# Kernel tuning notes

Hardware: AMD Instinct MI355X
Metric: run time of the kernel (lower is better)

Reference implementation:

```python
import jax, jax.numpy as jnp
import numpy as np


def setup_inputs() -> dict:
    key = jax.random.key(0)
    ks = jax.random.split(key, 6)
    B, HW, CIN, COUT, K = 256, 64, 3, 128, 32
    inputs = jax.random.normal(ks[0], (B, HW, HW, CIN), jnp.float32)
    conv_w = jax.random.normal(ks[1], (3, 3, CIN, COUT), jnp.float32) * 0.1
    conv_b = jnp.zeros((COUT,), jnp.float32)
    match_w = jax.random.normal(ks[2], (COUT,), jnp.float32) * 0.1
    match_b = jnp.zeros((1,), jnp.float32)
    pat_w = jax.random.normal(ks[3], (32 * 32 * K, 1), jnp.float32) * 0.01
    pat_b = jnp.zeros((1,), jnp.float32)
    base_w = jax.random.normal(ks[4], (32 * 32 * COUT, 3), jnp.float32) * 0.01
    base_b = jnp.zeros((3,), jnp.float32)
    pattern_set_index = jax.random.randint(ks[5], (K,), 0, COUT, jnp.int32)
    return {
        "inputs": inputs, "conv_w": conv_w, "conv_b": conv_b,
        "match_w": match_w, "match_b": match_b,
        "pat_w": pat_w, "pat_b": pat_b,
        "base_w": base_w, "base_b": base_b,
        "pattern_set_index": pattern_set_index,
    }


def reference(inputs, conv_w, conv_b, match_w, match_b,
              pat_w, pat_b, base_w, base_b, pattern_set_index):
    B = inputs.shape[0]
    # feat_extract: conv3x3 stride 2 + relu -> feats0 [B,32,32,128]; GAP -> feats1 [B,128]
    feats0 = jax.nn.relu(
        jax.lax.conv_general_dilated(
            inputs, conv_w, window_strides=(2, 2), padding='SAME',
            dimension_numbers=('NHWC', 'HWIO', 'NHWC')) + conv_b)
    feats1 = feats0.mean(axis=(1, 2))  # [B,128]
    # pat_matcher: boolean per-sample match mask
    matches = (feats1 @ match_w + match_b[0]) > 0.0  # [B] bool
    # pat_pred on channel-subset features (tf.gather axis=3)
    sel = jnp.take(feats0, pattern_set_index, axis=3)  # [B,32,32,32]
    p = jax.nn.sigmoid(sel.reshape(B, -1) @ pat_w + pat_b)[:, 0]  # [B]
    # BinaryToCategorical(pattern_class=0, num_classes=3): [p, (1-p)/2, (1-p)/2]
    o = (1.0 - p) * 0.5
    cat = jnp.stack([p, o, o], axis=-1)  # [B,3]
    # base_pred on full features (used for matched-low and non-matched samples)
    base = jax.nn.softmax(feats0.reshape(B, -1) @ base_w + base_b, axis=-1)  # [B,3]
    # route: matched AND pat score >= 0.5 -> categorized pat pred, else base pred
    use_pat = matches & (p >= 0.5)
    return jnp.where(use_pat[:, None], cat, base)
```

## Files before the change

### kernel.cpp

```cpp
#include <hip/hip_runtime.h>
#include <math.h>

typedef float v2f __attribute__((ext_vector_type(2)));

__device__ float4 g_wqt[131072];
__device__ v2f g_cwt[64 * 29];

__global__ __launch_bounds__(256)
void prep_weights(const float* __restrict__ base_w,
                  const float* __restrict__ pat_w,
                  const int*   __restrict__ psi,
                  const float* __restrict__ conv_w,
                  const float* __restrict__ conv_b,
                  const float* __restrict__ match_w)
{
    int idx = blockIdx.x * 256 + threadIdx.x;
    int c = idx >> 10, hw = idx & 1023;
    const float* bp = base_w + ((size_t)hw * 128 + c) * 3;
    float pc = 0.f;
    const float* pr = pat_w + hw * 32;
    #pragma unroll
    for (int k = 0; k < 32; ++k)
        pc += (psi[k] == c) ? pr[k] : 0.f;
    g_wqt[idx] = make_float4(bp[0], bp[1], bp[2], pc);

    if (idx < 64 * 29) {
        int p = idx / 29, r = idx - p * 29;
        v2f v;
        if (r < 27)       v = (v2f){ conv_w[r * 128 + 2 * p], conv_w[r * 128 + 2 * p + 1] };
        else if (r == 27) v = (v2f){ conv_b[2 * p], conv_b[2 * p + 1] };
        else              v = (v2f){ match_w[2 * p], match_w[2 * p + 1] };
        g_cwt[idx] = v;
    }
}

__global__ __launch_bounds__(1024, 4)
void pattern_branch_kernel(const float* __restrict__ in,
                           const float* __restrict__ match_b,
                           const float* __restrict__ pat_b,
                           const float* __restrict__ base_b,
                           float* __restrict__ out)
{
    __shared__ float xf[65 * 200];
    __shared__ float red[16][5];

    const int b   = blockIdx.x;
    const int tid = threadIdx.x;

    float4* x4 = (float4*)xf;
    for (int s = tid; s < 65 * 50; s += 1024) x4[s] = make_float4(0.f, 0.f, 0.f, 0.f);
    __syncthreads();
    const float4* inp4 = (const float4*)(in + (size_t)b * 12288);
    for (int s = tid; s < 64 * 48; s += 1024) {
        int r = s / 48;
        int q = s - r * 48;
        x4[r * 50 + q] = inp4[s];
    }
    __syncthreads();

    const int oh = tid >> 5;
    const int ow = tid & 31;
    v2f xs[15];
    #pragma unroll
    for (int kh = 0; kh < 3; ++kh) {
        int rowoff = (2 * oh + kh) * 200 + 6 * ow;
        #pragma unroll
        for (int u = 0; u < 5; ++u)
            xs[kh * 5 + u] = *(const v2f*)&xf[rowoff + 2 * u];
    }

    v2f sm2  = (v2f){0.f, 0.f};
    v2f sb01 = (v2f){0.f, 0.f};
    v2f sb2p = (v2f){0.f, 0.f};

    for (int p = 0; p < 64; ++p) {
        const v2f* wp = g_cwt + p * 29;
        v2f accA = wp[27];
        v2f accB = (v2f){0.f, 0.f};
        #pragma unroll
        for (int kh = 0; kh < 3; ++kh)
            #pragma unroll
            for (int t9 = 0; t9 < 9; ++t9) {
                float xv = xs[kh * 5 + (t9 >> 1)][t9 & 1];
                v2f wv = wp[kh * 9 + t9];
                if (t9 & 1) accB = __builtin_elementwise_fma((v2f){xv, xv}, wv, accB);
                else        accA = __builtin_elementwise_fma((v2f){xv, xv}, wv, accA);
            }
        v2f f2 = __builtin_elementwise_max(accA + accB, (v2f){0.f, 0.f});

        float4 wv0 = g_wqt[(2 * p) * 1024 + tid];
        float4 wv1 = g_wqt[(2 * p + 1) * 1024 + tid];
        v2f mw2 = wp[28];
        sm2  = __builtin_elementwise_fma(mw2, f2, sm2);
        sb01 = __builtin_elementwise_fma((v2f){f2.x, f2.x}, (v2f){wv0.x, wv0.y}, sb01);
        sb01 = __builtin_elementwise_fma((v2f){f2.y, f2.y}, (v2f){wv1.x, wv1.y}, sb01);
        sb2p = __builtin_elementwise_fma((v2f){f2.x, f2.x}, (v2f){wv0.z, wv0.w}, sb2p);
        sb2p = __builtin_elementwise_fma((v2f){f2.y, f2.y}, (v2f){wv1.z, wv1.w}, sb2p);
    }

    float vals[5] = { sm2.x + sm2.y, sb01.x, sb01.y, sb2p.x, sb2p.y };
    #pragma unroll
    for (int off = 32; off > 0; off >>= 1)
        #pragma unroll
        for (int v = 0; v < 5; ++v)
            vals[v] += __shfl_down(vals[v], off, 64);
    int wv = tid >> 6, lane = tid & 63;
    if (lane == 0) {
        #pragma unroll
        for (int v = 0; v < 5; ++v) red[wv][v] = vals[v];
    }
    __syncthreads();
    if (tid == 0) {
        float t[5] = {0.f, 0.f, 0.f, 0.f, 0.f};
        for (int wj = 0; wj < 16; ++wj)
            #pragma unroll
            for (int v = 0; v < 5; ++v) t[v] += red[wj][v];
        float score = t[0] * (1.f / 1024.f) + match_b[0];
        float p = 1.f / (1.f + expf(-(t[4] + pat_b[0])));
        float l0 = t[1] + base_b[0], l1 = t[2] + base_b[1], l2 = t[3] + base_b[2];
        float m = fmaxf(l0, fmaxf(l1, l2));
        float e0 = expf(l0 - m), e1 = expf(l1 - m), e2 = expf(l2 - m);
        float inv = 1.f / (e0 + e1 + e2);
        bool use_pat = (score > 0.f) && (p >= 0.5f);
        float o0, o1, o2;
        if (use_pat) { o0 = p; o1 = 0.5f * (1.f - p); o2 = o1; }
        else         { o0 = e0 * inv; o1 = e1 * inv; o2 = e2 * inv; }
        out[b * 3 + 0] = o0;
        out[b * 3 + 1] = o1;
        out[b * 3 + 2] = o2;
    }
}

extern "C" void kernel_launch(void* const* d_in, const int* in_sizes, int n_in,
                              void* d_out, int out_size, void* d_ws, size_t ws_size,
                              hipStream_t stream) {
    const float* in      = (const float*)d_in[0];
    const float* conv_w  = (const float*)d_in[1];
    const float* conv_b  = (const float*)d_in[2];
    const float* match_w = (const float*)d_in[3];
    const float* match_b = (const float*)d_in[4];
    const float* pat_w   = (const float*)d_in[5];
    const float* pat_b   = (const float*)d_in[6];
    const float* base_w  = (const float*)d_in[7];
    const float* base_b  = (const float*)d_in[8];
    const int*   psi     = (const int*)d_in[9];
    float* out = (float*)d_out;

    (void)d_ws; (void)ws_size;

    prep_weights<<<512, 256, 0, stream>>>(base_w, pat_w, psi, conv_w, conv_b, match_w);

    int B = in_sizes[0] / (64 * 64 * 3);
    pattern_branch_kernel<<<B, 1024, 0, stream>>>(
        in, match_b, pat_b, base_b, out);
}
```

Measured before the change: 123.7 us.

## Split conv work by channel group across blocks and hold head weights in registers

Each of 256 blocks now handles 16 samples and one group of 8 output channels, not one sample and all 128 channels. This lets each thread keep its slice of the base/pattern head weights in registers and reuse it across the 16 samples, instead of re-reading the 2MB weight table once per sample. The next sample's input is prefetched into registers while the current one is computed. Per-group partial sums go to a global buffer and a new finish kernel reduces them and applies softmax/sigmoid routing. This adds a kernel launch and extra syncs, and the launch hardcodes 256 blocks, which assumes B=256.

```diff
diff --git a/kernel.cpp b/kernel.cpp
--- a/kernel.cpp
+++ b/kernel.cpp
@@ -5,6 +5,7 @@
 
 __device__ float4 g_wqt[131072];
 __device__ v2f g_cwt[64 * 29];
+__device__ float g_part[256 * 16 * 5];
 
 __global__ __launch_bounds__(256)
 void prep_weights(const float* __restrict__ base_w,
@@ -35,100 +36,148 @@
 }
 
 __global__ __launch_bounds__(1024, 4)
-void pattern_branch_kernel(const float* __restrict__ in,
-                           const float* __restrict__ match_b,
-                           const float* __restrict__ pat_b,
-                           const float* __restrict__ base_b,
-                           float* __restrict__ out)
+void pattern_branch_kernel(const float* __restrict__ in)
 {
     __shared__ float xf[65 * 200];
-    __shared__ float red[16][5];
-
-    const int b   = blockIdx.x;
+    __shared__ float red[16][16][5];
+
+    const int blk = blockIdx.x;
+    const int sg  = blk & 15;
+    const int cg  = blk >> 4;
+    const int b0  = sg * 16;
     const int tid = threadIdx.x;
+
+    float4 tA[4], tB[4];
+    #pragma unroll
+    for (int pp = 0; pp < 4; ++pp) {
+        int p = cg * 4 + pp;
+        tA[pp] = g_wqt[(2 * p) * 1024 + tid];
+        tB[pp] = g_wqt[(2 * p + 1) * 1024 + tid];
+    }
 
     float4* x4 = (float4*)xf;
     for (int s = tid; s < 65 * 50; s += 1024) x4[s] = make_float4(0.f, 0.f, 0.f, 0.f);
     __syncthreads();
-    const float4* inp4 = (const float4*)(in + (size_t)b * 12288);
-    for (int s = tid; s < 64 * 48; s += 1024) {
-        int r = s / 48;
-        int q = s - r * 48;
-        x4[r * 50 + q] = inp4[s];
+
+    {
+        const float4* ip = (const float4*)(in + (size_t)b0 * 12288);
+        #pragma unroll
+        for (int j = 0; j < 3; ++j) {
+            int s = tid + j * 1024;
+            int r = s / 48, q = s - r * 48;
+            x4[r * 50 + q] = ip[s];
+        }
     }
     __syncthreads();
 
     const int oh = tid >> 5;
     const int ow = tid & 31;
-    v2f xs[15];
-    #pragma unroll
-    for (int kh = 0; kh < 3; ++kh) {
-        int rowoff = (2 * oh + kh) * 200 + 6 * ow;
-        #pragma unroll
-        for (int u = 0; u < 5; ++u)
-            xs[kh * 5 + u] = *(const v2f*)&xf[rowoff + 2 * u];
-    }
-
-    v2f sm2  = (v2f){0.f, 0.f};
-    v2f sb01 = (v2f){0.f, 0.f};
-    v2f sb2p = (v2f){0.f, 0.f};
-
-    for (int p = 0; p < 64; ++p) {
-        const v2f* wp = g_cwt + p * 29;
-        v2f accA = wp[27];
-        v2f accB = (v2f){0.f, 0.f};
-        #pragma unroll
-        for (int kh = 0; kh < 3; ++kh)
-            #pragma unroll
-            for (int t9 = 0; t9 < 9; ++t9) {
-                float xv = xs[kh * 5 + (t9 >> 1)][t9 & 1];
-                v2f wv = wp[kh * 9 + t9];
-                if (t9 & 1) accB = __builtin_elementwise_fma((v2f){xv, xv}, wv, accB);
-                else        accA = __builtin_elementwise_fma((v2f){xv, xv}, wv, accA);
+
+    for (int smp = 0; smp < 16; ++smp) {
+        float4 pf[3];
+        if (smp < 15) {
+            const float4* ip = (const float4*)(in + (size_t)(b0 + smp + 1) * 12288);
+            #pragma unroll
+            for (int j = 0; j < 3; ++j) pf[j] = ip[tid + j * 1024];
+        }
+
+        v2f xs[15];
+        #pragma unroll
+        for (int kh = 0; kh < 3; ++kh) {
+            int rowoff = (2 * oh + kh) * 200 + 6 * ow;
+            #pragma unroll
+            for (int u = 0; u < 5; ++u)
+                xs[kh * 5 + u] = *(const v2f*)&xf[rowoff + 2 * u];
+        }
+
+        v2f sm2  = (v2f){0.f, 0.f};
+        v2f sb01 = (v2f){0.f, 0.f};
+        v2f sb2p = (v2f){0.f, 0.f};
+
+        #pragma unroll
+        for (int pp = 0; pp < 4; ++pp) {
+            const v2f* wp = g_cwt + (cg * 4 + pp) * 29;
+            v2f accA = wp[27];
+            v2f accB = (v2f){0.f, 0.f};
+            #pragma unroll
+            for (int kh = 0; kh < 3; ++kh)
+                #pragma unroll
+                for (int t9 = 0; t9 < 9; ++t9) {
+                    float xv = xs[kh * 5 + (t9 >> 1)][t9 & 1];
+                    v2f wv = wp[kh * 9 + t9];
+                    if (t9 & 1) accB = __builtin_elementwise_fma((v2f){xv, xv}, wv, accB);
+                    else        accA = __builtin_elementwise_fma((v2f){xv, xv}, wv, accA);
+                }
+            v2f f2 = __builtin_elementwise_max(accA + accB, (v2f){0.f, 0.f});
+
+            float4 wv0 = tA[pp];
+            float4 wv1 = tB[pp];
+            sm2  = __builtin_elementwise_fma(wp[28], f2, sm2);
+            sb01 = __builtin_elementwise_fma((v2f){f2.x, f2.x}, (v2f){wv0.x, wv0.y}, sb01);
+            sb01 = __builtin_elementwise_fma((v2f){f2.y, f2.y}, (v2f){wv1.x, wv1.y}, sb01);
+            sb2p = __builtin_elementwise_fma((v2f){f2.x, f2.x}, (v2f){wv0.z, wv0.w}, sb2p);
+            sb2p = __builtin_elementwise_fma((v2f){f2.y, f2.y}, (v2f){wv1.z, wv1.w}, sb2p);
+        }
+
+        float vals[5] = { sm2.x + sm2.y, sb01.x, sb01.y, sb2p.x, sb2p.y };
+        #pragma unroll
+        for (int off = 32; off > 0; off >>= 1)
+            #pragma unroll
+            for (int v = 0; v < 5; ++v)
+                vals[v] += __shfl_down(vals[v], off, 64);
+        if ((tid & 63) == 0) {
+            #pragma unroll
+            for (int v = 0; v < 5; ++v) red[smp][tid >> 6][v] = vals[v];
+        }
+
+        if (smp < 15) {
+            __syncthreads();
+            #pragma unroll
+            for (int j = 0; j < 3; ++j) {
+                int s = tid + j * 1024;
+                int r = s / 48, q = s - r * 48;
+                x4[r * 50 + q] = pf[j];
             }
-        v2f f2 = __builtin_elementwise_max(accA + accB, (v2f){0.f, 0.f});
-
-        float4 wv0 = g_wqt[(2 * p) * 1024 + tid];
-        float4 wv1 = g_wqt[(2 * p + 1) * 1024 + tid];
-        v2f mw2 = wp[28];
-        sm2  = __builtin_elementwise_fma(mw2, f2, sm2);
-        sb01 = __builtin_elementwise_fma((v2f){f2.x, f2.x}, (v2f){wv0.x, wv0.y}, sb01);
-        sb01 = __builtin_elementwise_fma((v2f){f2.y, f2.y}, (v2f){wv1.x, wv1.y}, sb01);
-        sb2p = __builtin_elementwise_fma((v2f){f2.x, f2.x}, (v2f){wv0.z, wv0.w}, sb2p);
-        sb2p = __builtin_elementwise_fma((v2f){f2.y, f2.y}, (v2f){wv1.z, wv1.w}, sb2p);
-    }
-
-    float vals[5] = { sm2.x + sm2.y, sb01.x, sb01.y, sb2p.x, sb2p.y };
-    #pragma unroll
-    for (int off = 32; off > 0; off >>= 1)
+            __syncthreads();
+        }
+    }
+
+    __syncthreads();
+    if (tid < 16 * 5) {
+        int s = tid / 5, v = tid - s * 5;
+        float t = 0.f;
+        #pragma unroll
+        for (int w = 0; w < 16; ++w) t += red[s][w][v];
+        g_part[((b0 + s) * 16 + cg) * 5 + v] = t;
+    }
+}
+
+__global__ __launch_bounds__(256)
+void finish_kernel(const float* __restrict__ match_b,
+                   const float* __restrict__ pat_b,
+                   const float* __restrict__ base_b,
+                   float* __restrict__ out, int B)
+{
+    int b = blockIdx.x * 256 + threadIdx.x;
+    if (b >= B) return;
+    float t[5] = {0.f, 0.f, 0.f, 0.f, 0.f};
+    for (int cg = 0; cg < 16; ++cg)
         #pragma unroll
         for (int v = 0; v < 5; ++v)
-            vals[v] += __shfl_down(vals[v], off, 64);
-    int wv = tid >> 6, lane = tid & 63;
-    if (lane == 0) {
-        #pragma unroll
-        for (int v = 0; v < 5; ++v) red[wv][v] = vals[v];
-    }
-    __syncthreads();
-    if (tid == 0) {
-        float t[5] = {0.f, 0.f, 0.f, 0.f, 0.f};
-        for (int wj = 0; wj < 16; ++wj)
-            #pragma unroll
-            for (int v = 0; v < 5; ++v) t[v] += red[wj][v];
-        float score = t[0] * (1.f / 1024.f) + match_b[0];
-        float p = 1.f / (1.f + expf(-(t[4] + pat_b[0])));
-        float l0 = t[1] + base_b[0], l1 = t[2] + base_b[1], l2 = t[3] + base_b[2];
-        float m = fmaxf(l0, fmaxf(l1, l2));
-        float e0 = expf(l0 - m), e1 = expf(l1 - m), e2 = expf(l2 - m);
-        float inv = 1.f / (e0 + e1 + e2);
-        bool use_pat = (score > 0.f) && (p >= 0.5f);
-        float o0, o1, o2;
-        if (use_pat) { o0 = p; o1 = 0.5f * (1.f - p); o2 = o1; }
-        else         { o0 = e0 * inv; o1 = e1 * inv; o2 = e2 * inv; }
-        out[b * 3 + 0] = o0;
-        out[b * 3 + 1] = o1;
-        out[b * 3 + 2] = o2;
-    }
+            t[v] += g_part[(b * 16 + cg) * 5 + v];
+    float score = t[0] * (1.f / 1024.f) + match_b[0];
+    float p = 1.f / (1.f + expf(-(t[4] + pat_b[0])));
+    float l0 = t[1] + base_b[0], l1 = t[2] + base_b[1], l2 = t[3] + base_b[2];
+    float m = fmaxf(l0, fmaxf(l1, l2));
+    float e0 = expf(l0 - m), e1 = expf(l1 - m), e2 = expf(l2 - m);
+    float inv = 1.f / (e0 + e1 + e2);
+    bool use_pat = (score > 0.f) && (p >= 0.5f);
+    float o0, o1, o2;
+    if (use_pat) { o0 = p; o1 = 0.5f * (1.f - p); o2 = o1; }
+    else         { o0 = e0 * inv; o1 = e1 * inv; o2 = e2 * inv; }
+    out[b * 3 + 0] = o0;
+    out[b * 3 + 1] = o1;
+    out[b * 3 + 2] = o2;
 }
 
 extern "C" void kernel_launch(void* const* d_in, const int* in_sizes, int n_in,
@@ -150,7 +199,8 @@
 
     prep_weights<<<512, 256, 0, stream>>>(base_w, pat_w, psi, conv_w, conv_b, match_w);
 
+    pattern_branch_kernel<<<256, 1024, 0, stream>>>(in);
+
     int B = in_sizes[0] / (64 * 64 * 3);
-    pattern_branch_kernel<<<B, 1024, 0, stream>>>(
-        in, match_b, pat_b, base_b, out);
-}
+    finish_kernel<<<(B + 255) / 256, 256, 0, stream>>>(match_b, pat_b, base_b, out, B);
+}
```

Measured after the change: 254.2 us. 105% more time.

## Tile by output row across sample groups, caching weights in LDS

Applied to the files above, without the earlier changes.

The work is restructured so each block handles one output row for a group of 16 samples instead of one whole sample. The row's base/pattern weight slice (128 channels × 32 columns) is staged once in shared memory and reused across all 16 samples, replacing per-sample global reads of the full weight table. Input rows are double-buffered two samples at a time, and channels are split across waves. Partial sums go to a global buffer and a new finish kernel reduces them, at the cost of an extra launch and hardcoded assumptions that B is a multiple of 16 and at most 256 (the size of g_part).

```diff
diff --git a/kernel.cpp b/kernel.cpp
--- a/kernel.cpp
+++ b/kernel.cpp
@@ -5,6 +5,7 @@
 
 __device__ float4 g_wqt[131072];
 __device__ v2f g_cwt[64 * 29];
+__device__ float g_part[256 * 32 * 5];
 
 __global__ __launch_bounds__(256)
 void prep_weights(const float* __restrict__ base_w,
@@ -35,100 +36,138 @@
 }
 
 __global__ __launch_bounds__(1024, 4)
-void pattern_branch_kernel(const float* __restrict__ in,
-                           const float* __restrict__ match_b,
-                           const float* __restrict__ pat_b,
-                           const float* __restrict__ base_b,
-                           float* __restrict__ out)
+void pattern_branch_kernel(const float* __restrict__ in)
 {
-    __shared__ float xf[65 * 200];
-    __shared__ float red[16][5];
+    __shared__ float4 tbl[128 * 32];
+    __shared__ float  xb[4 * 636];
+    __shared__ float  red[16][16][5];
 
-    const int b   = blockIdx.x;
+    const int blk = blockIdx.x;
+    const int g   = blk & 15;
+    const int rb  = blk >> 4;
+    const int b0  = g * 16;
     const int tid = threadIdx.x;
 
-    float4* x4 = (float4*)xf;
-    for (int s = tid; s < 65 * 50; s += 1024) x4[s] = make_float4(0.f, 0.f, 0.f, 0.f);
+    #pragma unroll
+    for (int j = 0; j < 4; ++j) {
+        int idx = j * 1024 + tid;
+        tbl[idx] = g_wqt[(idx >> 5) * 1024 + rb * 32 + (idx & 31)];
+    }
+    for (int s = tid; s < 4 * 636; s += 1024) xb[s] = 0.f;
     __syncthreads();
-    const float4* inp4 = (const float4*)(in + (size_t)b * 12288);
-    for (int s = tid; s < 64 * 48; s += 1024) {
-        int r = s / 48;
-        int q = s - r * 48;
-        x4[r * 50 + q] = inp4[s];
+
+    if (tid < 288) {
+        int sp = tid / 144, s2 = tid - sp * 144;
+        int r3 = s2 / 48, q = s2 - r3 * 48;
+        int gr = 2 * rb + r3;
+        if (gr < 64)
+            *(float4*)&xb[sp * 636 + r3 * 212 + q * 4] =
+                ((const float4*)(in + (size_t)(b0 + sp) * 12288))[gr * 48 + q];
     }
     __syncthreads();
 
-    const int oh = tid >> 5;
-    const int ow = tid & 31;
-    v2f xs[15];
-    #pragma unroll
-    for (int kh = 0; kh < 3; ++kh) {
-        int rowoff = (2 * oh + kh) * 200 + 6 * ow;
-        #pragma unroll
-        for (int u = 0; u < 5; ++u)
-            xs[kh * 5 + u] = *(const v2f*)&xf[rowoff + 2 * u];
-    }
+    const int px   = tid & 31;
+    const int h    = (tid >> 5) & 1;
+    const int wvid = tid >> 6;
+    const int lane = tid & 63;
 
-    v2f sm2  = (v2f){0.f, 0.f};
-    v2f sb01 = (v2f){0.f, 0.f};
-    v2f sb2p = (v2f){0.f, 0.f};
+    for (int it = 0; it < 8; ++it) {
+        if (it < 7 && tid < 288) {
+            int sp = tid / 144, s2 = tid - sp * 144;
+            int r3 = s2 / 48, q = s2 - r3 * 48;
+            int gr = 2 * rb + r3;
+            if (gr < 64)
+                *(float4*)&xb[(((it + 1) & 1) * 2 + sp) * 636 + r3 * 212 + q * 4] =
+                    ((const float4*)(in + (size_t)(b0 + 2 * it + 2 + sp) * 12288))[gr * 48 + q];
+        }
 
-    for (int p = 0; p < 64; ++p) {
-        const v2f* wp = g_cwt + p * 29;
-        v2f accA = wp[27];
-        v2f accB = (v2f){0.f, 0.f};
+        const float* xbase = &xb[((it & 1) * 2 + h) * 636];
+        v2f xs[15];
         #pragma unroll
         for (int kh = 0; kh < 3; ++kh)
             #pragma unroll
-            for (int t9 = 0; t9 < 9; ++t9) {
-                float xv = xs[kh * 5 + (t9 >> 1)][t9 & 1];
-                v2f wv = wp[kh * 9 + t9];
-                if (t9 & 1) accB = __builtin_elementwise_fma((v2f){xv, xv}, wv, accB);
-                else        accA = __builtin_elementwise_fma((v2f){xv, xv}, wv, accA);
-            }
-        v2f f2 = __builtin_elementwise_max(accA + accB, (v2f){0.f, 0.f});
+            for (int u = 0; u < 5; ++u)
+                xs[kh * 5 + u] = *(const v2f*)&xbase[kh * 212 + 6 * px + 2 * u];
 
-        float4 wv0 = g_wqt[(2 * p) * 1024 + tid];
-        float4 wv1 = g_wqt[(2 * p + 1) * 1024 + tid];
-        v2f mw2 = wp[28];
-        sm2  = __builtin_elementwise_fma(mw2, f2, sm2);
-        sb01 = __builtin_elementwise_fma((v2f){f2.x, f2.x}, (v2f){wv0.x, wv0.y}, sb01);
-        sb01 = __builtin_elementwise_fma((v2f){f2.y, f2.y}, (v2f){wv1.x, wv1.y}, sb01);
-        sb2p = __builtin_elementwise_fma((v2f){f2.x, f2.x}, (v2f){wv0.z, wv0.w}, sb2p);
-        sb2p = __builtin_elementwise_fma((v2f){f2.y, f2.y}, (v2f){wv1.z, wv1.w}, sb2p);
+        v2f sm2  = (v2f){0.f, 0.f};
+        v2f sb01 = (v2f){0.f, 0.f};
+        v2f sb2p = (v2f){0.f, 0.f};
+
+        #pragma unroll
+        for (int j = 0; j < 4; ++j) {
+            int p = wvid * 4 + j;
+            const v2f* wp = g_cwt + p * 29;
+            v2f accA = wp[27];
+            v2f accB = (v2f){0.f, 0.f};
+            #pragma unroll
+            for (int kh = 0; kh < 3; ++kh)
+                #pragma unroll
+                for (int t9 = 0; t9 < 9; ++t9) {
+                    float xv = xs[kh * 5 + (t9 >> 1)][t9 & 1];
+                    v2f wv = wp[kh * 9 + t9];
+                    if (t9 & 1) accB = __builtin_elementwise_fma((v2f){xv, xv}, wv, accB);
+                    else        accA = __builtin_elementwise_fma((v2f){xv, xv}, wv, accA);
+                }
+            v2f f2 = __builtin_elementwise_max(accA + accB, (v2f){0.f, 0.f});
+
+            float4 wv0 = tbl[(2 * p) * 32 + px];
+            float4 wv1 = tbl[(2 * p + 1) * 32 + px];
+            sm2  = __builtin_elementwise_fma(wp[28], f2, sm2);
+            sb01 = __builtin_elementwise_fma((v2f){f2.x, f2.x}, (v2f){wv0.x, wv0.y}, sb01);
+            sb01 = __builtin_elementwise_fma((v2f){f2.y, f2.y}, (v2f){wv1.x, wv1.y}, sb01);
+            sb2p = __builtin_elementwise_fma((v2f){f2.x, f2.x}, (v2f){wv0.z, wv0.w}, sb2p);
+            sb2p = __builtin_elementwise_fma((v2f){f2.y, f2.y}, (v2f){wv1.z, wv1.w}, sb2p);
+        }
+
+        float vals[5] = { sm2.x + sm2.y, sb01.x, sb01.y, sb2p.x, sb2p.y };
+        #pragma unroll
+        for (int m = 1; m <= 16; m <<= 1)
+            #pragma unroll
+            for (int v = 0; v < 5; ++v)
+                vals[v] += __shfl_xor(vals[v], m, 64);
+        if (lane == 0 || lane == 32) {
+            #pragma unroll
+            for (int v = 0; v < 5; ++v) red[2 * it + h][wvid][v] = vals[v];
+        }
+
+        __syncthreads();
     }
 
-    float vals[5] = { sm2.x + sm2.y, sb01.x, sb01.y, sb2p.x, sb2p.y };
-    #pragma unroll
-    for (int off = 32; off > 0; off >>= 1)
+    if (tid < 16 * 5) {
+        int s = tid / 5, v = tid - s * 5;
+        float t = 0.f;
+        #pragma unroll
+        for (int w = 0; w < 16; ++w) t += red[s][w][v];
+        g_part[((b0 + s) * 32 + rb) * 5 + v] = t;
+    }
+}
+
+__global__ __launch_bounds__(256)
+void finish_kernel(const float* __restrict__ match_b,
+                   const float* __restrict__ pat_b,
+                   const float* __restrict__ base_b,
+                   float* __restrict__ out, int B)
+{
+    int b = blockIdx.x * 256 + threadIdx.x;
+    if (b >= B) return;
+    float t[5] = {0.f, 0.f, 0.f, 0.f, 0.f};
+    for (int rb = 0; rb < 32; ++rb)
         #pragma unroll
         for (int v = 0; v < 5; ++v)
-            vals[v] += __shfl_down(vals[v], off, 64);
-    int wv = tid >> 6, lane = tid & 63;
-    if (lane == 0) {
-        #pragma unroll
-        for (int v = 0; v < 5; ++v) red[wv][v] = vals[v];
-    }
-    __syncthreads();
-    if (tid == 0) {
-        float t[5] = {0.f, 0.f, 0.f, 0.f, 0.f};
-        for (int wj = 0; wj < 16; ++wj)
-            #pragma unroll
-            for (int v = 0; v < 5; ++v) t[v] += red[wj][v];
-        float score = t[0] * (1.f / 1024.f) + match_b[0];
-        float p = 1.f / (1.f + expf(-(t[4] + pat_b[0])));
-        float l0 = t[1] + base_b[0], l1 = t[2] + base_b[1], l2 = t[3] + base_b[2];
-        float m = fmaxf(l0, fmaxf(l1, l2));
-        float e0 = expf(l0 - m), e1 = expf(l1 - m), e2 = expf(l2 - m);
-        float inv = 1.f / (e0 + e1 + e2);
-        bool use_pat = (score > 0.f) && (p >= 0.5f);
-        float o0, o1, o2;
-        if (use_pat) { o0 = p; o1 = 0.5f * (1.f - p); o2 = o1; }
-        else         { o0 = e0 * inv; o1 = e1 * inv; o2 = e2 * inv; }
-        out[b * 3 + 0] = o0;
-        out[b * 3 + 1] = o1;
-        out[b * 3 + 2] = o2;
-    }
+            t[v] += g_part[(b * 32 + rb) * 5 + v];
+    float score = t[0] * (1.f / 1024.f) + match_b[0];
+    float p = 1.f / (1.f + expf(-(t[4] + pat_b[0])));
+    float l0 = t[1] + base_b[0], l1 = t[2] + base_b[1], l2 = t[3] + base_b[2];
+    float m = fmaxf(l0, fmaxf(l1, l2));
+    float e0 = expf(l0 - m), e1 = expf(l1 - m), e2 = expf(l2 - m);
+    float inv = 1.f / (e0 + e1 + e2);
+    bool use_pat = (score > 0.f) && (p >= 0.5f);
+    float o0, o1, o2;
+    if (use_pat) { o0 = p; o1 = 0.5f * (1.f - p); o2 = o1; }
+    else         { o0 = e0 * inv; o1 = e1 * inv; o2 = e2 * inv; }
+    out[b * 3 + 0] = o0;
+    out[b * 3 + 1] = o1;
+    out[b * 3 + 2] = o2;
 }
 
 extern "C" void kernel_launch(void* const* d_in, const int* in_sizes, int n_in,
@@ -151,6 +190,6 @@
     prep_weights<<<512, 256, 0, stream>>>(base_w, pat_w, psi, conv_w, conv_b, match_w);
 
     int B = in_sizes[0] / (64 * 64 * 3);
-    pattern_branch_kernel<<<B, 1024, 0, stream>>>(
-        in, match_b, pat_b, base_b, out);
+    pattern_branch_kernel<<<32 * (B / 16), 1024, 0, stream>>>(in);
+    finish_kernel<<<(B + 255) / 256, 256, 0, stream>>>(match_b, pat_b, base_b, out, B);
 }
```

Result: slower. 215.1 us (+73.9%).
